# Kernel tuning notes

Hardware: AMD Instinct MI355X
Metric: run time of the kernel (lower is better)

Reference implementation:

```python
import jax, jax.numpy as jnp
import numpy as np
from jax import lax

NUM_HEADS = 4
DIM = 192
EPS = 1e-12  # torch F.normalize eps


def setup_inputs() -> dict:
    key = jax.random.key(0)
    ks = jax.random.split(key, 5)
    b, c, h, w = 8, DIM, 128, 128
    x = jax.random.normal(ks[0], (b, c, h, w), dtype=jnp.float32)
    f = jax.random.normal(ks[1], (b, c, h, w), dtype=jnp.float32)
    # conv weights, scaled like kaiming-ish init
    w_qkv = jax.random.normal(ks[2], (3 * c, c, 1, 1), dtype=jnp.float32) * (1.0 / np.sqrt(c))
    w_dw = jax.random.normal(ks[3], (3 * c, 1, 3, 3), dtype=jnp.float32) * (1.0 / 3.0)
    w_proj = jax.random.normal(ks[4], (c, c, 1, 1), dtype=jnp.float32) * (1.0 / np.sqrt(c))
    temperature = jnp.ones((NUM_HEADS, 1, 1), dtype=jnp.float32)
    return {"x": x, "f": f, "w_qkv": w_qkv, "w_dw": w_dw, "w_proj": w_proj,
            "temperature": temperature}


def _conv(x, w, groups=1):
    return lax.conv_general_dilated(
        x, w, window_strides=(1, 1), padding="SAME",
        dimension_numbers=("NCHW", "OIHW", "NCHW"),
        feature_group_count=groups)


def reference(x, f, w_qkv, w_dw, w_proj, temperature):
    b, c, h, w = x.shape
    x_in = x + f
    qkv = _conv(x_in, w_qkv)                 # [b, 3c, h, w] 1x1 conv
    qkv = _conv(qkv, w_dw, groups=3 * c)     # depthwise 3x3
    q, k, v = jnp.split(qkv, 3, axis=1)      # each [b, c, h, w]
    hw = h * w
    ch = c // NUM_HEADS

    def heads(t):
        return t.reshape(b, NUM_HEADS, ch, hw)  # 'b (head c) h w -> b head c (h w)'

    q, k, v = heads(q), heads(k), heads(v)
    # L2-normalize over spatial (last) dim, torch-style eps clamp
    q = q / jnp.maximum(jnp.linalg.norm(q, axis=-1, keepdims=True), EPS)
    k = k / jnp.maximum(jnp.linalg.norm(k, axis=-1, keepdims=True), EPS)
    # transposed (channel) attention: [b, head, ch, ch]
    attn = jnp.einsum("bhcn,bhdn->bhcd", q, k) * temperature[None]
    attn = jax.nn.softmax(attn, axis=-1)
    out = jnp.einsum("bhcd,bhdn->bhcn", attn, v)  # [b, head, ch, hw]
    out = out.reshape(b, c, h, w)
    return _conv(out, w_proj)
```

## Files before the change

kernel.cpp:

```cpp
#include <hip/hip_runtime.h>
#include <stdint.h>

#define NB 8
#define NC 192
#define NOC 576
#define NH 4
#define HW 16384
#define NCHUNK 16

typedef unsigned short u16;
typedef __bf16 v8bf __attribute__((ext_vector_type(8)));
typedef float v4f __attribute__((ext_vector_type(4)));
typedef u16 v8us __attribute__((ext_vector_type(8)));
typedef u16 v4us __attribute__((ext_vector_type(4)));

__device__ __forceinline__ u16 f2bf(float f) {
    uint32_t u = __float_as_uint(f);
    u += 0x7FFFu + ((u >> 16) & 1u);
    return (u16)(u >> 16);
}
__device__ __forceinline__ float bf2f(u16 u) {
    return __uint_as_float(((uint32_t)u) << 16);
}

__global__ void k_cvt_w(const float* __restrict__ w, u16* __restrict__ wb, int n) {
    int i = blockIdx.x * 256 + threadIdx.x;
    if (i < n) wb[i] = f2bf(w[i]);
}

__global__ __launch_bounds__(512, 4) void k_gemm_qkv(
    const float* __restrict__ x, const float* __restrict__ f,
    const u16* __restrict__ wb, u16* __restrict__ qkv, int b0)
{
    __shared__ u16 smem[36864];
    u16* bt = smem;
    u16* wt = smem + 12288;
    const int t = threadIdx.x;
    const int bl = blockIdx.y;
    const int bg = b0 + bl;
    const int pblk = blockIdx.x;
    const int p0 = pblk * 64;

    {
        const int px = t & 63;
        const int cg = t >> 6;
        #pragma unroll
        for (int it = 0; it < 3; ++it) {
            const int c4 = it * 8 + cg;
            const size_t base = ((size_t)bg * NC + c4 * 8) * HW + p0 + px;
            v8us pk;
            #pragma unroll
            for (int j = 0; j < 8; ++j) {
                float v = x[base + (size_t)j * HW] + f[base + (size_t)j * HW];
                pk[j] = f2bf(v);
            }
            *reinterpret_cast<v8us*>(&bt[px * 192 + ((c4 ^ (px & 7)) << 3)]) = pk;
        }
    }

    const int w = t >> 6, l = t & 63, lr = l & 15, lg = l >> 4;
    const int wp = w >> 2;
    const int wo = w & 3;
    const int oc0 = wo * 144;

    v4f acc[2][9];
    #pragma unroll
    for (int mi = 0; mi < 2; ++mi)
        #pragma unroll
        for (int ni = 0; ni < 9; ++ni)
            acc[mi][ni] = (v4f){0.f, 0.f, 0.f, 0.f};

    v8us wload[5];
    #pragma unroll
    for (int it = 0; it < 5; ++it) {
        const int idx = it * 512 + t;
        if (idx < 2304) {
            const int oc = idx >> 2, q = idx & 3;
            wload[it] = *reinterpret_cast<const v8us*>(&wb[oc * 192 + q * 8]);
        }
    }

    #pragma unroll 1
    for (int ks = 0; ks < 6; ++ks) {
        __syncthreads();
        #pragma unroll
        for (int it = 0; it < 5; ++it) {
            const int idx = it * 512 + t;
            if (idx < 2304) {
                const int oc = idx >> 2, q = idx & 3;
                const int g = (oc ^ (oc >> 2)) & 3;
                *reinterpret_cast<v8us*>(&wt[oc * 32 + ((q ^ g) << 3)]) = wload[it];
            }
        }
        if (ks < 5) {
            #pragma unroll
            for (int it = 0; it < 5; ++it) {
                const int idx = it * 512 + t;
                if (idx < 2304) {
                    const int oc = idx >> 2, q = idx & 3;
                    wload[it] = *reinterpret_cast<const v8us*>(&wb[oc * 192 + (ks + 1) * 32 + q * 8]);
                }
            }
        }
        __syncthreads();

        v8bf a[2];
        #pragma unroll
        for (int mi = 0; mi < 2; ++mi) {
            const int px = wp * 32 + mi * 16 + lr;
            a[mi] = *reinterpret_cast<const v8bf*>(&bt[px * 192 + (((ks * 4 + lg) ^ (px & 7)) << 3)]);
        }
        #pragma unroll
        for (int ni = 0; ni < 9; ++ni) {
            const int oc = oc0 + ni * 16 + lr;
            const int g = (oc ^ (oc >> 2)) & 3;
            const v8bf bw = *reinterpret_cast<const v8bf*>(&wt[oc * 32 + ((lg ^ g) << 3)]);
            #pragma unroll
            for (int mi = 0; mi < 2; ++mi)
                acc[mi][ni] = __builtin_amdgcn_mfma_f32_16x16x32_bf16(a[mi], bw, acc[mi][ni], 0, 0, 0);
        }
    }

    __syncthreads();
    u16* et = smem;
    #pragma unroll
    for (int mi = 0; mi < 2; ++mi)
        #pragma unroll
        for (int ni = 0; ni < 9; ++ni) {
            const int oc = oc0 + ni * 16 + lr;
            const int u = wp * 8 + mi * 4 + lg;
            const int su = u ^ (oc & 15);
            v4us pk;
            pk[0] = f2bf(acc[mi][ni][0]); pk[1] = f2bf(acc[mi][ni][1]);
            pk[2] = f2bf(acc[mi][ni][2]); pk[3] = f2bf(acc[mi][ni][3]);
            *reinterpret_cast<v4us*>(&et[oc * 64 + su * 4]) = pk;
        }
    __syncthreads();
    const size_t obase = ((size_t)bl * 256 + pblk) * 36864;
    #pragma unroll
    for (int rd = 0; rd < 9; ++rd) {
        const int idx = rd * 512 + t;
        const int oc = idx >> 3;
        const int ck = idx & 7;
        const int u0 = (ck * 2) ^ (oc & 15);
        const int u1 = (ck * 2 + 1) ^ (oc & 15);
        v4us lo = *reinterpret_cast<v4us*>(&et[oc * 64 + u0 * 4]);
        v4us hi = *reinterpret_cast<v4us*>(&et[oc * 64 + u1 * 4]);
        v8us o8;
        o8[0] = lo[0]; o8[1] = lo[1]; o8[2] = lo[2]; o8[3] = lo[3];
        o8[4] = hi[0]; o8[5] = hi[1]; o8[6] = hi[2]; o8[7] = hi[3];
        *reinterpret_cast<v8us*>(&qkv[obase + (size_t)idx * 8]) = o8;
    }
}

__global__ __launch_bounds__(256) void k_dw(
    const u16* __restrict__ qkv, const float* __restrict__ wdw,
    u16* __restrict__ qk_out, u16* __restrict__ v_out,
    float* __restrict__ sumsq, int b0)
{
    __shared__ u16 plane[128 * 136];
    __shared__ float red[4];
    const int t = threadIdx.x;
    const int ch = blockIdx.x;
    const int bl = blockIdx.y;
    const int bg = b0 + bl;

    float wk[9];
    #pragma unroll
    for (int i = 0; i < 9; ++i) wk[i] = wdw[ch * 9 + i];

    const int r = t >> 1;
    const int cb = (t & 1) * 64;

    {
        const u16* src = qkv + ((size_t)bl * 256) * 36864 + (size_t)ch * 64;
        #pragma unroll
        for (int i = 0; i < 8; ++i) {
            const int e = i * 2048 + t * 8;
            const int pblk = e >> 6, px = e & 63;
            v8us v = *reinterpret_cast<const v8us*>(&src[(size_t)pblk * 36864 + px]);
            const int rr = e >> 7, cc = e & 127;
            *reinterpret_cast<v8us*>(&plane[rr * 136 + cc]) = v;
        }
    }
    __syncthreads();

    const bool vm = (r > 0), vp = (r < 127);
    const u16* rowm = &plane[(r - 1) * 136];
    const u16* rowc = &plane[r * 136];
    const u16* rowp = &plane[(r + 1) * 136];

    float am, ac, bm, bc, cm, cc2;
    if (cb == 0) { am = 0.f; bm = 0.f; cm = 0.f; }
    else {
        am = vm ? bf2f(rowm[cb - 1]) : 0.f;
        bm = bf2f(rowc[cb - 1]);
        cm = vp ? bf2f(rowp[cb - 1]) : 0.f;
    }
    ac = vm ? bf2f(rowm[cb]) : 0.f;
    bc = bf2f(rowc[cb]);
    cc2 = vp ? bf2f(rowp[cb]) : 0.f;

    uint32_t ov[32];
    float ssq = 0.f;
    #pragma unroll
    for (int xp = 0; xp < 32; ++xp) {
        #pragma unroll
        for (int s2 = 0; s2 < 2; ++s2) {
            const int col = cb + xp * 2 + s2;
            float ap, bp, cp;
            if (col < 127) {
                ap = vm ? bf2f(rowm[col + 1]) : 0.f;
                bp = bf2f(rowc[col + 1]);
                cp = vp ? bf2f(rowp[col + 1]) : 0.f;
            } else { ap = 0.f; bp = 0.f; cp = 0.f; }
            float o = wk[0]*am + wk[1]*ac + wk[2]*ap
                    + wk[3]*bm + wk[4]*bc + wk[5]*bp
                    + wk[6]*cm + wk[7]*cc2 + wk[8]*cp;
            u16 ob = f2bf(o);
            float orr = bf2f(ob);
            ssq += orr * orr;
            ov[xp] = (s2 == 0) ? (uint32_t)ob : (ov[xp] | ((uint32_t)ob << 16));
            am = ac; ac = ap; bm = bc; bc = bp; cm = cc2; cc2 = cp;
        }
    }

    __syncthreads();
    #pragma unroll
    for (int i = 0; i < 32; ++i)
        *reinterpret_cast<uint32_t*>(&plane[r * 136 + cb + i * 2]) = ov[i];
    __syncthreads();

    u16* dst = (ch < 2 * NC) ? (qk_out + ((size_t)bg * (2 * NC) + ch) * HW)
                             : (v_out + ((size_t)bg * NC + (ch - 2 * NC)) * HW);
    #pragma unroll
    for (int i = 0; i < 8; ++i) {
        const int idx = i * 2048 + t * 8;
        const int rr = idx >> 7, cc = idx & 127;
        v8us v = *reinterpret_cast<const v8us*>(&plane[rr * 136 + cc]);
        *reinterpret_cast<v8us*>(&dst[idx]) = v;
    }

    #pragma unroll
    for (int off = 32; off > 0; off >>= 1) ssq += __shfl_down(ssq, off);
    if ((t & 63) == 0) red[t >> 6] = ssq;
    __syncthreads();
    if (t == 0 && ch < 2 * NC) sumsq[bg * (2 * NC) + ch] = red[0] + red[1] + red[2] + red[3];
}

__global__ __launch_bounds__(256) void k_attn(
    const u16* __restrict__ qk, float* __restrict__ partials)
{
    __shared__ float wsum[4 * 2304];
    const int t = threadIdx.x;
    const int chunk = blockIdx.x;
    const int h = blockIdx.y;
    const int b = blockIdx.z;
    const int w = t >> 6, l = t & 63, lr = l & 15, lg = l >> 4;

    const size_t qbase = ((size_t)b * 384 + h * 48) * HW;
    const size_t kbase = ((size_t)b * 384 + 192 + h * 48) * HW;
    const int pb = chunk * 1024 + w * 256;

    v4f acc[3][3];
    #pragma unroll
    for (int mi = 0; mi < 3; ++mi)
        #pragma unroll
        for (int ni = 0; ni < 3; ++ni)
            acc[mi][ni] = (v4f){0.f, 0.f, 0.f, 0.f};

    #pragma unroll
    for (int ks = 0; ks < 8; ++ks) {
        const int k = pb + ks * 32 + lg * 8;
        v8bf a[3], bb[3];
        #pragma unroll
        for (int mi = 0; mi < 3; ++mi)
            a[mi] = *reinterpret_cast<const v8bf*>(&qk[qbase + (size_t)(mi * 16 + lr) * HW + k]);
        #pragma unroll
        for (int ni = 0; ni < 3; ++ni)
            bb[ni] = *reinterpret_cast<const v8bf*>(&qk[kbase + (size_t)(ni * 16 + lr) * HW + k]);
        #pragma unroll
        for (int mi = 0; mi < 3; ++mi)
            #pragma unroll
            for (int ni = 0; ni < 3; ++ni)
                acc[mi][ni] = __builtin_amdgcn_mfma_f32_16x16x32_bf16(a[mi], bb[ni], acc[mi][ni], 0, 0, 0);
    }

    #pragma unroll
    for (int mi = 0; mi < 3; ++mi)
        #pragma unroll
        for (int ni = 0; ni < 3; ++ni)
            #pragma unroll
            for (int r = 0; r < 4; ++r)
                wsum[w * 2304 + (mi * 16 + lg * 4 + r) * 48 + ni * 16 + lr] = acc[mi][ni][r];
    __syncthreads();

    #pragma unroll
    for (int i = 0; i < 9; ++i) {
        const int e = t + i * 256;
        float s = wsum[e] + wsum[2304 + e] + wsum[4608 + e] + wsum[6912 + e];
        partials[(((size_t)(b * NH + h)) * NCHUNK + chunk) * 2304 + e] = s;
    }
}

__global__ __launch_bounds__(256) void k_smx(
    const float* __restrict__ partials, const float* __restrict__ sumsq,
    const float* __restrict__ wproj, const float* __restrict__ temp,
    u16* __restrict__ Mb)
{
    __shared__ float att[2304];
    __shared__ float rq[48], rk[48];
    const int t = threadIdx.x;
    const int h = blockIdx.x;
    const int b = blockIdx.y;

    if (t < 48) {
        float s = sumsq[b * 384 + h * 48 + t];
        rq[t] = 1.f / fmaxf(sqrtf(s), 1e-12f);
    } else if (t < 96) {
        float s = sumsq[b * 384 + 192 + h * 48 + (t - 48)];
        rk[t - 48] = 1.f / fmaxf(sqrtf(s), 1e-12f);
    }
    __syncthreads();
    const float tp = temp[h];
    #pragma unroll
    for (int i = 0; i < 9; ++i) {
        const int e = t + i * 256;
        const float* pp = &partials[(((size_t)(b * NH + h)) * NCHUNK) * 2304 + e];
        float s = 0.f;
        #pragma unroll
        for (int c = 0; c < NCHUNK; ++c) s += pp[(size_t)c * 2304];
        att[e] = s * rq[e / 48] * rk[e % 48] * tp;
    }
    __syncthreads();
    if (t < 48) {
        float m = -1e30f;
        #pragma unroll
        for (int j = 0; j < 48; ++j) m = fmaxf(m, att[t * 48 + j]);
        float s = 0.f;
        for (int j = 0; j < 48; ++j) { float e2 = __expf(att[t * 48 + j] - m); att[t * 48 + j] = e2; s += e2; }
        const float inv = 1.f / s;
        for (int j = 0; j < 48; ++j) att[t * 48 + j] *= inv;
    }
    __syncthreads();
    #pragma unroll
    for (int i = 0; i < 36; ++i) {
        const int idx = t + i * 256;
        const int oc = idx / 48, d = idx % 48;
        float s = 0.f;
        #pragma unroll
        for (int cc = 0; cc < 48; ++cc)
            s += wproj[oc * 192 + h * 48 + cc] * att[cc * 48 + d];
        Mb[((size_t)b * NC + oc) * NC + h * 48 + d] = f2bf(s);
    }
}

__global__ __launch_bounds__(256) void k_gemm_out(
    const u16* __restrict__ vp, const u16* __restrict__ Mb,
    float* __restrict__ out)
{
    __shared__ u16 bt[64 * 192];
    const int t = threadIdx.x;
    const int b = blockIdx.y;
    const int p0 = blockIdx.x * 64;

    {
        const int px = t & 63;
        const int cg = t >> 6;
        #pragma unroll
        for (int it = 0; it < 6; ++it) {
            const int c4 = it * 4 + cg;
            const size_t base = ((size_t)b * NC + c4 * 8) * HW + p0 + px;
            v8us pk;
            #pragma unroll
            for (int j = 0; j < 8; ++j) pk[j] = vp[base + (size_t)j * HW];
            *reinterpret_cast<v8us*>(&bt[px * 192 + ((c4 ^ (px & 7)) << 3)]) = pk;
        }
    }
    __syncthreads();

    const int w = t >> 6, l = t & 63, lr = l & 15, lg = l >> 4;
    const int oc0 = w * 48;

    v4f acc[4][3];
    #pragma unroll
    for (int mi = 0; mi < 4; ++mi)
        #pragma unroll
        for (int ni = 0; ni < 3; ++ni)
            acc[mi][ni] = (v4f){0.f, 0.f, 0.f, 0.f};

    #pragma unroll
    for (int ks = 0; ks < 6; ++ks) {
        const int k = ks * 32 + lg * 8;
        const int c4 = ks * 4 + lg;
        v8bf a[4];
        #pragma unroll
        for (int mi = 0; mi < 4; ++mi) {
            const int px = mi * 16 + lr;
            a[mi] = *reinterpret_cast<const v8bf*>(&bt[px * 192 + ((c4 ^ (px & 7)) << 3)]);
        }
        #pragma unroll
        for (int ni = 0; ni < 3; ++ni) {
            const int oc = oc0 + ni * 16 + lr;
            const v8bf bw = *reinterpret_cast<const v8bf*>(&Mb[((size_t)b * NC + oc) * NC + k]);
            #pragma unroll
            for (int mi = 0; mi < 4; ++mi)
                acc[mi][ni] = __builtin_amdgcn_mfma_f32_16x16x32_bf16(a[mi], bw, acc[mi][ni], 0, 0, 0);
        }
    }

    #pragma unroll
    for (int mi = 0; mi < 4; ++mi)
        #pragma unroll
        for (int ni = 0; ni < 3; ++ni) {
            const int oc = oc0 + ni * 16 + lr;
            const int px = p0 + mi * 16 + lg * 4;
            *reinterpret_cast<v4f*>(&out[((size_t)b * NC + oc) * HW + px]) = acc[mi][ni];
        }
}

extern "C" void kernel_launch(void* const* d_in, const int* in_sizes, int n_in,
                              void* d_out, int out_size, void* d_ws, size_t ws_size,
                              hipStream_t stream)
{
    (void)in_sizes; (void)n_in; (void)out_size;
    const float* x      = (const float*)d_in[0];
    const float* f      = (const float*)d_in[1];
    const float* w_qkv  = (const float*)d_in[2];
    const float* w_dw   = (const float*)d_in[3];
    const float* w_proj = (const float*)d_in[4];
    const float* temp   = (const float*)d_in[5];

    char* ws = (char*)d_ws;
    u16*   vws      = (u16*)(ws);
    u16*   wb       = (u16*)(ws + 50331648);
    float* sumsq    = (float*)(ws + 50552832);
    float* partials = (float*)(ws + 50565120);
    u16*   Mb       = (u16*)(ws + 55283712);
    const size_t FIXED = 55873536;
    const size_t PERB  = (size_t)NOC * HW * 2;
    u16*   qkv_raw  = (u16*)(ws + FIXED);

    int g = 1;
    if (ws_size > FIXED + PERB) {
        size_t avail = (ws_size - FIXED) / PERB;
        g = (int)(avail > 8 ? 8 : avail);
        if (g < 1) g = 1;
    }

    u16* qk_scratch = (u16*)d_out;
    float* out      = (float*)d_out;

    hipLaunchKernelGGL(k_cvt_w, dim3(432), dim3(256), 0, stream, w_qkv, wb, NOC * NC);
    for (int b0 = 0; b0 < NB; b0 += g) {
        const int nb = (b0 + g <= NB) ? g : (NB - b0);
        hipLaunchKernelGGL(k_gemm_qkv, dim3(HW / 64, nb), dim3(512), 0, stream, x, f, wb, qkv_raw, b0);
        hipLaunchKernelGGL(k_dw, dim3(NOC, nb), dim3(256), 0, stream, qkv_raw, w_dw, qk_scratch, vws, sumsq, b0);
    }
    hipLaunchKernelGGL(k_attn, dim3(NCHUNK, NH, NB), dim3(256), 0, stream, qk_scratch, partials);
    hipLaunchKernelGGL(k_smx, dim3(NH, NB), dim3(256), 0, stream, partials, sumsq, w_proj, temp, Mb);
    hipLaunchKernelGGL(k_gemm_out, dim3(HW / 64, NB), dim3(256), 0, stream, vws, Mb, out);
}
```

Measured before the change: 295.2 us.

## Enlarge QKV GEMM tile to 128 pixels, widen depthwise blocks, stage output stores

The QKV GEMM block now covers 128 pixels with 1024 threads, so each weight k-slice staged in shared memory is reused across twice as many pixels. The epilogue writes the two 64-pixel halves in two passes through shared memory. The depthwise kernel moves to 512 threads, each handling 32 columns, with wider 16-byte shared stores. The output GEMM now stages its accumulators through a swizzled shared tile so global stores are contiguous rows. In exchange, the larger blocks use more LDS and registers per block and may lower occupancy.

```diff
diff --git a/kernel.cpp b/kernel.cpp
--- a/kernel.cpp
+++ b/kernel.cpp
@@ -28,22 +28,21 @@
     if (i < n) wb[i] = f2bf(w[i]);
 }
 
-__global__ __launch_bounds__(512, 4) void k_gemm_qkv(
+__global__ __launch_bounds__(1024) void k_gemm_qkv(
     const float* __restrict__ x, const float* __restrict__ f,
     const u16* __restrict__ wb, u16* __restrict__ qkv, int b0)
 {
-    __shared__ u16 smem[36864];
+    __shared__ u16 smem[43008];
     u16* bt = smem;
-    u16* wt = smem + 12288;
+    u16* wt = smem + 24576;
     const int t = threadIdx.x;
     const int bl = blockIdx.y;
     const int bg = b0 + bl;
-    const int pblk = blockIdx.x;
-    const int p0 = pblk * 64;
+    const int p0 = blockIdx.x * 128;
 
     {
-        const int px = t & 63;
-        const int cg = t >> 6;
+        const int px = t & 127;
+        const int cg = t >> 7;
         #pragma unroll
         for (int it = 0; it < 3; ++it) {
             const int c4 = it * 8 + cg;
@@ -70,10 +69,10 @@
         for (int ni = 0; ni < 9; ++ni)
             acc[mi][ni] = (v4f){0.f, 0.f, 0.f, 0.f};
 
-    v8us wload[5];
-    #pragma unroll
-    for (int it = 0; it < 5; ++it) {
-        const int idx = it * 512 + t;
+    v8us wload[3];
+    #pragma unroll
+    for (int it = 0; it < 3; ++it) {
+        const int idx = it * 1024 + t;
         if (idx < 2304) {
             const int oc = idx >> 2, q = idx & 3;
             wload[it] = *reinterpret_cast<const v8us*>(&wb[oc * 192 + q * 8]);
@@ -84,8 +83,8 @@
     for (int ks = 0; ks < 6; ++ks) {
         __syncthreads();
         #pragma unroll
-        for (int it = 0; it < 5; ++it) {
-            const int idx = it * 512 + t;
+        for (int it = 0; it < 3; ++it) {
+            const int idx = it * 1024 + t;
             if (idx < 2304) {
                 const int oc = idx >> 2, q = idx & 3;
                 const int g = (oc ^ (oc >> 2)) & 3;
@@ -94,8 +93,8 @@
         }
         if (ks < 5) {
             #pragma unroll
-            for (int it = 0; it < 5; ++it) {
-                const int idx = it * 512 + t;
+            for (int it = 0; it < 3; ++it) {
+                const int idx = it * 1024 + t;
                 if (idx < 2304) {
                     const int oc = idx >> 2, q = idx & 3;
                     wload[it] = *reinterpret_cast<const v8us*>(&wb[oc * 192 + (ks + 1) * 32 + q * 8]);
@@ -121,45 +120,52 @@
         }
     }
 
-    __syncthreads();
     u16* et = smem;
     #pragma unroll
-    for (int mi = 0; mi < 2; ++mi)
-        #pragma unroll
-        for (int ni = 0; ni < 9; ++ni) {
-            const int oc = oc0 + ni * 16 + lr;
-            const int u = wp * 8 + mi * 4 + lg;
-            const int su = u ^ (oc & 15);
-            v4us pk;
-            pk[0] = f2bf(acc[mi][ni][0]); pk[1] = f2bf(acc[mi][ni][1]);
-            pk[2] = f2bf(acc[mi][ni][2]); pk[3] = f2bf(acc[mi][ni][3]);
-            *reinterpret_cast<v4us*>(&et[oc * 64 + su * 4]) = pk;
-        }
-    __syncthreads();
-    const size_t obase = ((size_t)bl * 256 + pblk) * 36864;
-    #pragma unroll
-    for (int rd = 0; rd < 9; ++rd) {
-        const int idx = rd * 512 + t;
-        const int oc = idx >> 3;
-        const int ck = idx & 7;
-        const int u0 = (ck * 2) ^ (oc & 15);
-        const int u1 = (ck * 2 + 1) ^ (oc & 15);
-        v4us lo = *reinterpret_cast<v4us*>(&et[oc * 64 + u0 * 4]);
-        v4us hi = *reinterpret_cast<v4us*>(&et[oc * 64 + u1 * 4]);
-        v8us o8;
-        o8[0] = lo[0]; o8[1] = lo[1]; o8[2] = lo[2]; o8[3] = lo[3];
-        o8[4] = hi[0]; o8[5] = hi[1]; o8[6] = hi[2]; o8[7] = hi[3];
-        *reinterpret_cast<v8us*>(&qkv[obase + (size_t)idx * 8]) = o8;
-    }
-}
-
-__global__ __launch_bounds__(256) void k_dw(
+    for (int pass = 0; pass < 2; ++pass) {
+        __syncthreads();
+        if ((wp >> 1) == pass) {
+            #pragma unroll
+            for (int mi = 0; mi < 2; ++mi)
+                #pragma unroll
+                for (int ni = 0; ni < 9; ++ni) {
+                    const int oc = oc0 + ni * 16 + lr;
+                    const int u = (wp & 1) * 8 + mi * 4 + lg;
+                    const int su = u ^ (oc & 15);
+                    v4us pk;
+                    pk[0] = f2bf(acc[mi][ni][0]); pk[1] = f2bf(acc[mi][ni][1]);
+                    pk[2] = f2bf(acc[mi][ni][2]); pk[3] = f2bf(acc[mi][ni][3]);
+                    *reinterpret_cast<v4us*>(&et[oc * 64 + su * 4]) = pk;
+                }
+        }
+        __syncthreads();
+        const size_t obase = ((size_t)bl * 256 + blockIdx.x * 2 + pass) * 36864;
+        #pragma unroll
+        for (int rd = 0; rd < 5; ++rd) {
+            const int idx = rd * 1024 + t;
+            if (idx < 4608) {
+                const int oc = idx >> 3;
+                const int ck = idx & 7;
+                const int u0 = (ck * 2) ^ (oc & 15);
+                const int u1 = (ck * 2 + 1) ^ (oc & 15);
+                v4us lo = *reinterpret_cast<v4us*>(&et[oc * 64 + u0 * 4]);
+                v4us hi = *reinterpret_cast<v4us*>(&et[oc * 64 + u1 * 4]);
+                v8us o8;
+                o8[0] = lo[0]; o8[1] = lo[1]; o8[2] = lo[2]; o8[3] = lo[3];
+                o8[4] = hi[0]; o8[5] = hi[1]; o8[6] = hi[2]; o8[7] = hi[3];
+                *reinterpret_cast<v8us*>(&qkv[obase + (size_t)idx * 8]) = o8;
+            }
+        }
+    }
+}
+
+__global__ __launch_bounds__(512) void k_dw(
     const u16* __restrict__ qkv, const float* __restrict__ wdw,
     u16* __restrict__ qk_out, u16* __restrict__ v_out,
     float* __restrict__ sumsq, int b0)
 {
     __shared__ u16 plane[128 * 136];
-    __shared__ float red[4];
+    __shared__ float red[8];
     const int t = threadIdx.x;
     const int ch = blockIdx.x;
     const int bl = blockIdx.y;
@@ -169,14 +175,14 @@
     #pragma unroll
     for (int i = 0; i < 9; ++i) wk[i] = wdw[ch * 9 + i];
 
-    const int r = t >> 1;
-    const int cb = (t & 1) * 64;
+    const int r = t >> 2;
+    const int cq = (t & 3) * 32;
 
     {
         const u16* src = qkv + ((size_t)bl * 256) * 36864 + (size_t)ch * 64;
         #pragma unroll
-        for (int i = 0; i < 8; ++i) {
-            const int e = i * 2048 + t * 8;
+        for (int i = 0; i < 4; ++i) {
+            const int e = i * 4096 + t * 8;
             const int pblk = e >> 6, px = e & 63;
             v8us v = *reinterpret_cast<const v8us*>(&src[(size_t)pblk * 36864 + px]);
             const int rr = e >> 7, cc = e & 127;
@@ -191,23 +197,23 @@
     const u16* rowp = &plane[(r + 1) * 136];
 
     float am, ac, bm, bc, cm, cc2;
-    if (cb == 0) { am = 0.f; bm = 0.f; cm = 0.f; }
+    if (cq == 0) { am = 0.f; bm = 0.f; cm = 0.f; }
     else {
-        am = vm ? bf2f(rowm[cb - 1]) : 0.f;
-        bm = bf2f(rowc[cb - 1]);
-        cm = vp ? bf2f(rowp[cb - 1]) : 0.f;
-    }
-    ac = vm ? bf2f(rowm[cb]) : 0.f;
-    bc = bf2f(rowc[cb]);
-    cc2 = vp ? bf2f(rowp[cb]) : 0.f;
-
-    uint32_t ov[32];
+        am = vm ? bf2f(rowm[cq - 1]) : 0.f;
+        bm = bf2f(rowc[cq - 1]);
+        cm = vp ? bf2f(rowp[cq - 1]) : 0.f;
+    }
+    ac = vm ? bf2f(rowm[cq]) : 0.f;
+    bc = bf2f(rowc[cq]);
+    cc2 = vp ? bf2f(rowp[cq]) : 0.f;
+
+    uint32_t ov[16];
     float ssq = 0.f;
     #pragma unroll
-    for (int xp = 0; xp < 32; ++xp) {
+    for (int xp = 0; xp < 16; ++xp) {
         #pragma unroll
         for (int s2 = 0; s2 < 2; ++s2) {
-            const int col = cb + xp * 2 + s2;
+            const int col = cq + xp * 2 + s2;
             float ap, bp, cp;
             if (col < 127) {
                 ap = vm ? bf2f(rowm[col + 1]) : 0.f;
@@ -227,15 +233,19 @@
 
     __syncthreads();
     #pragma unroll
-    for (int i = 0; i < 32; ++i)
-        *reinterpret_cast<uint32_t*>(&plane[r * 136 + cb + i * 2]) = ov[i];
+    for (int k = 0; k < 4; ++k) {
+        uint4 w4;
+        w4.x = ov[k * 4 + 0]; w4.y = ov[k * 4 + 1];
+        w4.z = ov[k * 4 + 2]; w4.w = ov[k * 4 + 3];
+        *reinterpret_cast<uint4*>(&plane[r * 136 + cq + k * 8]) = w4;
+    }
     __syncthreads();
 
     u16* dst = (ch < 2 * NC) ? (qk_out + ((size_t)bg * (2 * NC) + ch) * HW)
                              : (v_out + ((size_t)bg * NC + (ch - 2 * NC)) * HW);
     #pragma unroll
-    for (int i = 0; i < 8; ++i) {
-        const int idx = i * 2048 + t * 8;
+    for (int i = 0; i < 4; ++i) {
+        const int idx = i * 4096 + t * 8;
         const int rr = idx >> 7, cc = idx & 127;
         v8us v = *reinterpret_cast<const v8us*>(&plane[rr * 136 + cc]);
         *reinterpret_cast<v8us*>(&dst[idx]) = v;
@@ -245,7 +255,12 @@
     for (int off = 32; off > 0; off >>= 1) ssq += __shfl_down(ssq, off);
     if ((t & 63) == 0) red[t >> 6] = ssq;
     __syncthreads();
-    if (t == 0 && ch < 2 * NC) sumsq[bg * (2 * NC) + ch] = red[0] + red[1] + red[2] + red[3];
+    if (t == 0 && ch < 2 * NC) {
+        float s = 0.f;
+        #pragma unroll
+        for (int i = 0; i < 8; ++i) s += red[i];
+        sumsq[bg * (2 * NC) + ch] = s;
+    }
 }
 
 __global__ __launch_bounds__(256) void k_attn(
@@ -359,7 +374,8 @@
     const u16* __restrict__ vp, const u16* __restrict__ Mb,
     float* __restrict__ out)
 {
-    __shared__ u16 bt[64 * 192];
+    __shared__ float smemf[12288];
+    u16* bt = reinterpret_cast<u16*>(smemf);
     const int t = threadIdx.x;
     const int b = blockIdx.y;
     const int p0 = blockIdx.x * 64;
@@ -409,14 +425,27 @@
         }
     }
 
+    __syncthreads();
+    float* et = smemf;
     #pragma unroll
     for (int mi = 0; mi < 4; ++mi)
         #pragma unroll
         for (int ni = 0; ni < 3; ++ni) {
             const int oc = oc0 + ni * 16 + lr;
-            const int px = p0 + mi * 16 + lg * 4;
-            *reinterpret_cast<v4f*>(&out[((size_t)b * NC + oc) * HW + px]) = acc[mi][ni];
-        }
+            const int u = mi * 4 + lg;
+            const int su = u ^ (oc & 15);
+            *reinterpret_cast<v4f*>(&et[oc * 64 + su * 4]) = acc[mi][ni];
+        }
+    __syncthreads();
+    #pragma unroll
+    for (int rd = 0; rd < 12; ++rd) {
+        const int idx = rd * 256 + t;
+        const int oc = idx >> 4;
+        const int u = idx & 15;
+        const int su = u ^ (oc & 15);
+        v4f v = *reinterpret_cast<v4f*>(&et[oc * 64 + su * 4]);
+        *reinterpret_cast<v4f*>(&out[((size_t)b * NC + oc) * HW + p0 + u * 4]) = v;
+    }
 }
 
 extern "C" void kernel_launch(void* const* d_in, const int* in_sizes, int n_in,
@@ -454,8 +483,8 @@
     hipLaunchKernelGGL(k_cvt_w, dim3(432), dim3(256), 0, stream, w_qkv, wb, NOC * NC);
     for (int b0 = 0; b0 < NB; b0 += g) {
         const int nb = (b0 + g <= NB) ? g : (NB - b0);
-        hipLaunchKernelGGL(k_gemm_qkv, dim3(HW / 64, nb), dim3(512), 0, stream, x, f, wb, qkv_raw, b0);
-        hipLaunchKernelGGL(k_dw, dim3(NOC, nb), dim3(256), 0, stream, qkv_raw, w_dw, qk_scratch, vws, sumsq, b0);
+        hipLaunchKernelGGL(k_gemm_qkv, dim3(HW / 128, nb), dim3(1024), 0, stream, x, f, wb, qkv_raw, b0);
+        hipLaunchKernelGGL(k_dw, dim3(NOC, nb), dim3(512), 0, stream, qkv_raw, w_dw, qk_scratch, vws, sumsq, b0);
     }
     hipLaunchKernelGGL(k_attn, dim3(NCHUNK, NH, NB), dim3(256), 0, stream, qk_scratch, partials);
     hipLaunchKernelGGL(k_smx, dim3(NH, NB), dim3(256), 0, stream, partials, sumsq, w_proj, temp, Mb);
```

New measurement: 285.2 us. 3.4% less time.
